# Kernel tuning notes

Measured on AMD Instinct MI355X. Metric: run time of the kernel, lower is better.

## Reference

```python
import jax, jax.numpy as jnp
import numpy as np

B, T, D, H, L = 8192, 80, 32, 64, 3


def setup_inputs() -> dict:
    key = jax.random.key(0)
    ks = jax.random.split(key, 16)
    s = lambda k, shape, fan: jax.random.normal(k, shape, jnp.float32) / np.sqrt(fan)
    inp = {"x": jax.random.normal(ks[0], (B, T, D), jnp.float32)}
    dims_in = [D, H, H]
    i = 1
    for l in range(L):
        din = dims_in[l]
        inp[f"W_ih{l}"] = s(ks[i], (H, din), H); i += 1
        inp[f"W_hh{l}"] = s(ks[i], (H, H), H); i += 1
        inp[f"b_ih{l}"] = s(ks[i], (H,), H); i += 1
        inp[f"b_hh{l}"] = s(ks[i], (H,), H); i += 1
    inp["W_fc"] = s(ks[i], (1, H), H); i += 1
    inp["b_fc"] = s(ks[i], (1,), H)
    return inp


def _rnn_layer(xs, W_ih, W_hh, b_ih, b_hh):
    # xs: [T, B, Din] -> ys: [T, B, H]; tanh RNN recurrence (PyTorch nn.RNN math)
    pre = jnp.einsum('tbd,hd->tbh', xs, W_ih) + b_ih + b_hh  # input proj precomputed
    h0 = jnp.zeros((xs.shape[1], W_hh.shape[0]), xs.dtype)
    def step(h, p):
        h_new = jnp.tanh(p + h @ W_hh.T)
        return h_new, h_new
    _, ys = jax.lax.scan(step, h0, pre)
    return ys


def reference(x, W_ih0, W_hh0, b_ih0, b_hh0, W_ih1, W_hh1, b_ih1, b_hh1,
              W_ih2, W_hh2, b_ih2, b_hh2, W_fc, b_fc):
    # x: [B, T, D] (batch_first) -> time-major [T, B, D]
    h = jnp.swapaxes(x, 0, 1)
    params = [(W_ih0, W_hh0, b_ih0, b_hh0),
              (W_ih1, W_hh1, b_ih1, b_hh1),
              (W_ih2, W_hh2, b_ih2, b_hh2)]
    for (W_ih, W_hh, b_ih, b_hh) in params:
        h = _rnn_layer(h, W_ih, W_hh, b_ih, b_hh)
    last = h[-1]                      # [B, H] == out[:, -1, :]
    return last @ W_fc.T + b_fc       # [B, 1]
```

## Files before the change

### kernel.cpp

```cpp
#include <hip/hip_runtime.h>
#include <hip/hip_bf16.h>
#include <cstddef>


typedef __attribute__((ext_vector_type(8))) short s16x8;
typedef __attribute__((ext_vector_type(4))) short s16x4;
typedef __attribute__((ext_vector_type(4))) float fx4;

#define MFMA16(A, B, C) __builtin_amdgcn_mfma_f32_16x16x32_bf16((A), (B), (C), 0, 0, 0)

#if __has_builtin(__builtin_amdgcn_exp2f)
#define EXP2F(x) __builtin_amdgcn_exp2f(x)
#else
#define EXP2F(x) exp2f(x)
#endif
#if __has_builtin(__builtin_amdgcn_rcpf)
#define RCPF(x) __builtin_amdgcn_rcpf(x)
#else
#define RCPF(x) (1.0f / (x))
#endif

static constexpr float K2LOG2E = 2.8853900817779268f;

__device__ __forceinline__ short f2bf(float f) {
  union { float f; unsigned u; } v; v.f = f;
  unsigned r = v.u + 0x7FFFu + ((v.u >> 16) & 1u);
  return (short)(r >> 16);
}
__device__ __forceinline__ float bf2f(short s) {
  union { unsigned u; float f; } v; v.u = ((unsigned)(unsigned short)s) << 16;
  return v.f;
}
__device__ __forceinline__ unsigned pk2bf(float a, float b) {
  float2 t; t.x = a; t.y = b;
  union { __hip_bfloat162 h; unsigned u; } c;
  c.h = __float22bfloat162_rn(t);
  return c.u;
}

__device__ __forceinline__ s16x8 wfragA(const float* W, int ncols, int row, int col0) {
  const float* p = W + row * ncols + col0;
  s16x8 r;
#pragma unroll
  for (int i = 0; i < 8; ++i) r[i] = f2bf(p[i]);
  return r;
}

__global__ __launch_bounds__(384, 3) void rnn3_pipe6(
    const float* __restrict__ x,
    const float* __restrict__ Wih0, const float* __restrict__ Whh0,
    const float* __restrict__ bih0, const float* __restrict__ bhh0,
    const float* __restrict__ Wih1, const float* __restrict__ Whh1,
    const float* __restrict__ bih1, const float* __restrict__ bhh1,
    const float* __restrict__ Wih2, const float* __restrict__ Whh2,
    const float* __restrict__ bih2, const float* __restrict__ bhh2,
    const float* __restrict__ Wfc, const float* __restrict__ bfc,
    float* __restrict__ out)
{
  __shared__ __align__(16) short hb[3][2][16][72];

  const int tid = threadIdx.x;
  const int wvu = __builtin_amdgcn_readfirstlane(tid >> 6);
  const int l   = wvu >> 1;
  const int s   = wvu & 1;
  const int ln  = tid & 63;
  const int q   = ln >> 4;
  const int m15 = ln & 15;
  const int bbase = (int)blockIdx.x * 16;

  const float* Wih = (l == 0) ? Wih0 : (l == 1) ? Wih1 : Wih2;
  const float* Whh = (l == 0) ? Whh0 : (l == 1) ? Whh1 : Whh2;
  const float* bi  = (l == 0) ? bih0 : (l == 1) ? bih1 : bih2;
  const float* bh  = (l == 0) ? bhh0 : (l == 1) ? bhh1 : bhh2;
  const int kin = (l == 0) ? 32 : 64;

  const s16x8 z8 = {0, 0, 0, 0, 0, 0, 0, 0};
  s16x8 wi0[2], wi1[2], whOwn[2], whOth[2];
#pragma unroll
  for (int tile = 0; tile < 2; ++tile) {
    const int row = 32 * s + 16 * tile + m15;
    wi0[tile]   = wfragA(Wih, kin, row, 8 * q);
    wi1[tile]   = l ? wfragA(Wih, 64, row, 32 + 8 * q) : z8;
    whOwn[tile] = wfragA(Whh, 64, row, 32 * s + 8 * q);
    whOth[tile] = wfragA(Whh, 64, row, 32 * (1 - s) + 8 * q);
  }

  float bsc[2][4];
#pragma unroll
  for (int tile = 0; tile < 2; ++tile)
#pragma unroll
    for (int r = 0; r < 4; ++r) {
      const int j = 32 * s + 16 * tile + 4 * q + r;
      bsc[tile][r] = (bi[j] + bh[j]) * K2LOG2E;
    }

  short*       wr_[2]  = {&hb[l][0][m15][32 * s + 4 * q], &hb[l][1][m15][32 * s + 4 * q]};
  const short* own_[2] = {&hb[l][0][m15][32 * s + 8 * q], &hb[l][1][m15][32 * s + 8 * q]};
  const short* oth_[2] = {&hb[l][0][m15][32 * (1 - s) + 8 * q],
                          &hb[l][1][m15][32 * (1 - s) + 8 * q]};
  const int lup = (l == 0) ? 0 : l - 1;
  const short* up_[2]  = {&hb[lup][0][m15][8 * q], &hb[lup][1][m15][8 * q]};

  const float* xr = x + (size_t)(bbase + m15) * (80 * 32) + 8 * q;
  fx4 xc0 = {0, 0, 0, 0}, xc1 = {0, 0, 0, 0};
  if (l == 0) { xc0 = *(const fx4*)(xr); xc1 = *(const fx4*)(xr + 4); }

  const fx4 z4 = {0.f, 0.f, 0.f, 0.f};
  s16x8 rOwn = z8;

  for (int tau = 0; tau < 82; ++tau) {
    const int lt = tau - l;
    if (0 <= lt && lt < 80) {
      const int p  = lt & 1;
      const int pm = p ^ 1;
      s16x8 rOth = z8;
      if (lt > 0) rOth = *(const s16x8*)(oth_[pm]);
      s16x8 in0, in1 = z8;
      if (l == 0) {
        union { unsigned u[4]; s16x8 v; } xp;
        xp.u[0] = pk2bf(xc0[0], xc0[1]); xp.u[1] = pk2bf(xc0[2], xc0[3]);
        xp.u[2] = pk2bf(xc1[0], xc1[1]); xp.u[3] = pk2bf(xc1[2], xc1[3]);
        in0 = xp.v;
        const int tn = (lt < 79) ? lt + 1 : 79;
        xc0 = *(const fx4*)(xr + tn * 32);
        xc1 = *(const fx4*)(xr + tn * 32 + 4);
      } else {
        const short* up = up_[p];
        in0 = *(const s16x8*)(up);
        in1 = *(const s16x8*)(up + 32);
      }
      fx4 acc[2];
#pragma unroll
      for (int tile = 0; tile < 2; ++tile) acc[tile] = MFMA16(whOwn[tile], rOwn, z4);
#pragma unroll
      for (int tile = 0; tile < 2; ++tile) acc[tile] = MFMA16(whOth[tile], rOth, acc[tile]);
#pragma unroll
      for (int tile = 0; tile < 2; ++tile) acc[tile] = MFMA16(wi0[tile], in0, acc[tile]);
      if (l) {
#pragma unroll
        for (int tile = 0; tile < 2; ++tile) acc[tile] = MFMA16(wi1[tile], in1, acc[tile]);
      }
      short* wb = wr_[p];
#pragma unroll
      for (int tile = 0; tile < 2; ++tile) {
        float h[4];
#pragma unroll
        for (int r = 0; r < 4; ++r) {
          float e = EXP2F(__builtin_fmaf(acc[tile][r], K2LOG2E, bsc[tile][r]));
          h[r] = __builtin_fmaf(-2.f, RCPF(e + 1.f), 1.f);
        }
        union { unsigned u[2]; s16x4 v; } pk;
        pk.u[0] = pk2bf(h[0], h[1]);
        pk.u[1] = pk2bf(h[2], h[3]);
        *(s16x4*)(wb + 16 * tile) = pk.v;
      }
      rOwn = *(const s16x8*)(own_[p]);
    }
    __syncthreads();
  }

  if (wvu == 4) {
    const short* f = &hb[2][1][m15][8 * q];
    s16x8 f0 = *(const s16x8*)(f);
    s16x8 f1 = *(const s16x8*)(f + 32);
    float sv = 0.f;
#pragma unroll
    for (int i = 0; i < 8; ++i) sv += bf2f(f0[i]) * Wfc[8 * q + i];
#pragma unroll
    for (int i = 0; i < 8; ++i) sv += bf2f(f1[i]) * Wfc[32 + 8 * q + i];
    sv += __shfl_xor(sv, 16, 64);
    sv += __shfl_xor(sv, 32, 64);
    if (ln < 16) out[bbase + ln] = sv + bfc[0];
  }
}

extern "C" void kernel_launch(void* const* d_in, const int* in_sizes, int n_in,
                              void* d_out, int out_size, void* d_ws, size_t ws_size,
                              hipStream_t stream) {
  const float* x    = (const float*)d_in[0];
  const float* Wih0 = (const float*)d_in[1];
  const float* Whh0 = (const float*)d_in[2];
  const float* bih0 = (const float*)d_in[3];
  const float* bhh0 = (const float*)d_in[4];
  const float* Wih1 = (const float*)d_in[5];
  const float* Whh1 = (const float*)d_in[6];
  const float* bih1 = (const float*)d_in[7];
  const float* bhh1 = (const float*)d_in[8];
  const float* Wih2 = (const float*)d_in[9];
  const float* Whh2 = (const float*)d_in[10];
  const float* bih2 = (const float*)d_in[11];
  const float* bhh2 = (const float*)d_in[12];
  const float* Wfc  = (const float*)d_in[13];
  const float* bfc  = (const float*)d_in[14];

  rnn3_pipe6<<<dim3(512), dim3(384), 0, stream>>>(
      x, Wih0, Whh0, bih0, bhh0, Wih1, Whh1, bih1, bhh1,
      Wih2, Whh2, bih2, bhh2, Wfc, bfc, (float*)d_out);
}
```

Measured before the change: 209.0 us.

## Run all three layers per wave in a wavefront-skewed systolic loop

Each wave used to own one layer's half of the hidden state. Now each wave holds the weights for all three layers and computes every layer's output columns for its half, skewed in time so layer l handles step tau-l. A block covers two 16-row batch groups with 256 threads, and the grid drops to 256 blocks with launch bounds (256,1). The final FC dot is fused in from register-held layer-2 outputs and reduced through shared memory. The aim is to fill each wave's serial dependency chain with independent MFMAs from other layers. The cost is much higher register pressure and fewer resident waves, which may leave the latency of the recurrence exposed.

```diff
diff --git a/kernel.cpp b/kernel.cpp
--- a/kernel.cpp
+++ b/kernel.cpp
@@ -27,10 +27,6 @@
   unsigned r = v.u + 0x7FFFu + ((v.u >> 16) & 1u);
   return (short)(r >> 16);
 }
-__device__ __forceinline__ float bf2f(short s) {
-  union { unsigned u; float f; } v; v.u = ((unsigned)(unsigned short)s) << 16;
-  return v.f;
-}
 __device__ __forceinline__ unsigned pk2bf(float a, float b) {
   float2 t; t.x = a; t.y = b;
   union { __hip_bfloat162 h; unsigned u; } c;
@@ -46,7 +42,22 @@
   return r;
 }
 
-__global__ __launch_bounds__(384, 3) void rnn3_pipe6(
+__device__ __forceinline__ void tanh_pack_store(const fx4 acc, const float* bs,
+                                                short* wp, float* hout) {
+  float h[4];
+#pragma unroll
+  for (int r = 0; r < 4; ++r) {
+    float e = EXP2F(__builtin_fmaf(acc[r], K2LOG2E, bs[r]));
+    h[r] = __builtin_fmaf(-2.f, RCPF(e + 1.f), 1.f);
+    if (hout) hout[r] = h[r];
+  }
+  union { unsigned u[2]; s16x4 v; } pk;
+  pk.u[0] = pk2bf(h[0], h[1]);
+  pk.u[1] = pk2bf(h[2], h[3]);
+  *(s16x4*)wp = pk.v;
+}
+
+__global__ __launch_bounds__(256, 1) void rnn3_sys(
     const float* __restrict__ x,
     const float* __restrict__ Wih0, const float* __restrict__ Whh0,
     const float* __restrict__ bih0, const float* __restrict__ bhh0,
@@ -57,121 +68,131 @@
     const float* __restrict__ Wfc, const float* __restrict__ bfc,
     float* __restrict__ out)
 {
-  __shared__ __align__(16) short hb[3][2][16][72];
+  __shared__ __align__(16) short hb[2][3][2][16][72];
 
   const int tid = threadIdx.x;
   const int wvu = __builtin_amdgcn_readfirstlane(tid >> 6);
-  const int l   = wvu >> 1;
+  const int g   = wvu >> 1;
   const int s   = wvu & 1;
   const int ln  = tid & 63;
   const int q   = ln >> 4;
   const int m15 = ln & 15;
-  const int bbase = (int)blockIdx.x * 16;
-
-  const float* Wih = (l == 0) ? Wih0 : (l == 1) ? Wih1 : Wih2;
-  const float* Whh = (l == 0) ? Whh0 : (l == 1) ? Whh1 : Whh2;
-  const float* bi  = (l == 0) ? bih0 : (l == 1) ? bih1 : bih2;
-  const float* bh  = (l == 0) ? bhh0 : (l == 1) ? bhh1 : bhh2;
-  const int kin = (l == 0) ? 32 : 64;
-
-  const s16x8 z8 = {0, 0, 0, 0, 0, 0, 0, 0};
-  s16x8 wi0[2], wi1[2], whOwn[2], whOth[2];
+  const int bbase = (int)blockIdx.x * 32 + g * 16;
+
+  {
+    const s16x8 z = {0, 0, 0, 0, 0, 0, 0, 0};
+    s16x8* pz = (s16x8*)&hb[0][0][0][0][0];
+    for (int i = tid; i < (int)(sizeof(hb) / 16); i += 256) pz[i] = z;
+  }
+
+  s16x8 wi0[2], wh0[2][2], wi1[2][2], wh1[2][2], wi2[2][2], wh2[2][2];
 #pragma unroll
   for (int tile = 0; tile < 2; ++tile) {
     const int row = 32 * s + 16 * tile + m15;
-    wi0[tile]   = wfragA(Wih, kin, row, 8 * q);
-    wi1[tile]   = l ? wfragA(Wih, 64, row, 32 + 8 * q) : z8;
-    whOwn[tile] = wfragA(Whh, 64, row, 32 * s + 8 * q);
-    whOth[tile] = wfragA(Whh, 64, row, 32 * (1 - s) + 8 * q);
-  }
-
-  float bsc[2][4];
+    wi0[tile] = wfragA(Wih0, 32, row, 8 * q);
+#pragma unroll
+    for (int kf = 0; kf < 2; ++kf) {
+      const int c = 32 * kf + 8 * q;
+      wh0[tile][kf] = wfragA(Whh0, 64, row, c);
+      wi1[tile][kf] = wfragA(Wih1, 64, row, c);
+      wh1[tile][kf] = wfragA(Whh1, 64, row, c);
+      wi2[tile][kf] = wfragA(Wih2, 64, row, c);
+      wh2[tile][kf] = wfragA(Whh2, 64, row, c);
+    }
+  }
+
+  float bs[3][2][4];
 #pragma unroll
   for (int tile = 0; tile < 2; ++tile)
 #pragma unroll
     for (int r = 0; r < 4; ++r) {
       const int j = 32 * s + 16 * tile + 4 * q + r;
-      bsc[tile][r] = (bi[j] + bh[j]) * K2LOG2E;
-    }
-
-  short*       wr_[2]  = {&hb[l][0][m15][32 * s + 4 * q], &hb[l][1][m15][32 * s + 4 * q]};
-  const short* own_[2] = {&hb[l][0][m15][32 * s + 8 * q], &hb[l][1][m15][32 * s + 8 * q]};
-  const short* oth_[2] = {&hb[l][0][m15][32 * (1 - s) + 8 * q],
-                          &hb[l][1][m15][32 * (1 - s) + 8 * q]};
-  const int lup = (l == 0) ? 0 : l - 1;
-  const short* up_[2]  = {&hb[lup][0][m15][8 * q], &hb[lup][1][m15][8 * q]};
+      bs[0][tile][r] = (bih0[j] + bhh0[j]) * K2LOG2E;
+      bs[1][tile][r] = (bih1[j] + bhh1[j]) * K2LOG2E;
+      bs[2][tile][r] = (bih2[j] + bhh2[j]) * K2LOG2E;
+    }
+
+  short* wrp[3][2];
+  const short* rdp[3][2];
+#pragma unroll
+  for (int l = 0; l < 3; ++l)
+#pragma unroll
+    for (int p = 0; p < 2; ++p) {
+      wrp[l][p] = &hb[g][l][p][m15][32 * s + 4 * q];
+      rdp[l][p] = &hb[g][l][p][m15][8 * q];
+    }
 
   const float* xr = x + (size_t)(bbase + m15) * (80 * 32) + 8 * q;
-  fx4 xc0 = {0, 0, 0, 0}, xc1 = {0, 0, 0, 0};
-  if (l == 0) { xc0 = *(const fx4*)(xr); xc1 = *(const fx4*)(xr + 4); }
+  fx4 xa = *(const fx4*)(xr);
+  fx4 xb = *(const fx4*)(xr + 4);
 
   const fx4 z4 = {0.f, 0.f, 0.f, 0.f};
-  s16x8 rOwn = z8;
+  float hk2[2][4];
+
+  __syncthreads();
 
   for (int tau = 0; tau < 82; ++tau) {
-    const int lt = tau - l;
-    if (0 <= lt && lt < 80) {
-      const int p  = lt & 1;
-      const int pm = p ^ 1;
-      s16x8 rOth = z8;
-      if (lt > 0) rOth = *(const s16x8*)(oth_[pm]);
-      s16x8 in0, in1 = z8;
-      if (l == 0) {
-        union { unsigned u[4]; s16x8 v; } xp;
-        xp.u[0] = pk2bf(xc0[0], xc0[1]); xp.u[1] = pk2bf(xc0[2], xc0[3]);
-        xp.u[2] = pk2bf(xc1[0], xc1[1]); xp.u[3] = pk2bf(xc1[2], xc1[3]);
-        in0 = xp.v;
-        const int tn = (lt < 79) ? lt + 1 : 79;
-        xc0 = *(const fx4*)(xr + tn * 32);
-        xc1 = *(const fx4*)(xr + tn * 32 + 4);
-      } else {
-        const short* up = up_[p];
-        in0 = *(const s16x8*)(up);
-        in1 = *(const s16x8*)(up + 32);
+    const int p  = tau & 1;
+    const int pm = p ^ 1;
+
+    s16x8 h0a = *(const s16x8*)(rdp[0][pm]);
+    s16x8 h0b = *(const s16x8*)(rdp[0][pm] + 32);
+    s16x8 h1a = *(const s16x8*)(rdp[1][pm]);
+    s16x8 h1b = *(const s16x8*)(rdp[1][pm] + 32);
+    s16x8 h2a = *(const s16x8*)(rdp[2][pm]);
+    s16x8 h2b = *(const s16x8*)(rdp[2][pm] + 32);
+
+    if (tau <= 79) {
+      union { unsigned u[4]; s16x8 v; } xp;
+      xp.u[0] = pk2bf(xa[0], xa[1]); xp.u[1] = pk2bf(xa[2], xa[3]);
+      xp.u[2] = pk2bf(xb[0], xb[1]); xp.u[3] = pk2bf(xb[2], xb[3]);
+      const int tn = (tau < 79) ? tau + 1 : 79;
+      xa = *(const fx4*)(xr + tn * 32);
+      xb = *(const fx4*)(xr + tn * 32 + 4);
+#pragma unroll
+      for (int tile = 0; tile < 2; ++tile) {
+        fx4 a = MFMA16(wi0[tile], xp.v, z4);
+        a = MFMA16(wh0[tile][0], h0a, a);
+        a = MFMA16(wh0[tile][1], h0b, a);
+        tanh_pack_store(a, bs[0][tile], wrp[0][p] + 16 * tile, nullptr);
       }
-      fx4 acc[2];
-#pragma unroll
-      for (int tile = 0; tile < 2; ++tile) acc[tile] = MFMA16(whOwn[tile], rOwn, z4);
-#pragma unroll
-      for (int tile = 0; tile < 2; ++tile) acc[tile] = MFMA16(whOth[tile], rOth, acc[tile]);
-#pragma unroll
-      for (int tile = 0; tile < 2; ++tile) acc[tile] = MFMA16(wi0[tile], in0, acc[tile]);
-      if (l) {
-#pragma unroll
-        for (int tile = 0; tile < 2; ++tile) acc[tile] = MFMA16(wi1[tile], in1, acc[tile]);
+    }
+    if (1 <= tau && tau <= 80) {
+#pragma unroll
+      for (int tile = 0; tile < 2; ++tile) {
+        fx4 a = MFMA16(wi1[tile][0], h0a, z4);
+        a = MFMA16(wi1[tile][1], h0b, a);
+        a = MFMA16(wh1[tile][0], h1a, a);
+        a = MFMA16(wh1[tile][1], h1b, a);
+        tanh_pack_store(a, bs[1][tile], wrp[1][p] + 16 * tile, nullptr);
       }
-      short* wb = wr_[p];
+    }
+    if (tau >= 2) {
 #pragma unroll
       for (int tile = 0; tile < 2; ++tile) {
-        float h[4];
-#pragma unroll
-        for (int r = 0; r < 4; ++r) {
-          float e = EXP2F(__builtin_fmaf(acc[tile][r], K2LOG2E, bsc[tile][r]));
-          h[r] = __builtin_fmaf(-2.f, RCPF(e + 1.f), 1.f);
-        }
-        union { unsigned u[2]; s16x4 v; } pk;
-        pk.u[0] = pk2bf(h[0], h[1]);
-        pk.u[1] = pk2bf(h[2], h[3]);
-        *(s16x4*)(wb + 16 * tile) = pk.v;
+        fx4 a = MFMA16(wi2[tile][0], h1a, z4);
+        a = MFMA16(wi2[tile][1], h1b, a);
+        a = MFMA16(wh2[tile][0], h2a, a);
+        a = MFMA16(wh2[tile][1], h2b, a);
+        tanh_pack_store(a, bs[2][tile], wrp[2][p] + 16 * tile, hk2[tile]);
       }
-      rOwn = *(const s16x8*)(own_[p]);
     }
     __syncthreads();
   }
 
-  if (wvu == 4) {
-    const short* f = &hb[2][1][m15][8 * q];
-    s16x8 f0 = *(const s16x8*)(f);
-    s16x8 f1 = *(const s16x8*)(f + 32);
-    float sv = 0.f;
-#pragma unroll
-    for (int i = 0; i < 8; ++i) sv += bf2f(f0[i]) * Wfc[8 * q + i];
-#pragma unroll
-    for (int i = 0; i < 8; ++i) sv += bf2f(f1[i]) * Wfc[32 + 8 * q + i];
-    sv += __shfl_xor(sv, 16, 64);
-    sv += __shfl_xor(sv, 32, 64);
-    if (ln < 16) out[bbase + ln] = sv + bfc[0];
-  }
+  float sv = 0.f;
+#pragma unroll
+  for (int tile = 0; tile < 2; ++tile)
+#pragma unroll
+    for (int r = 0; r < 4; ++r)
+      sv += hk2[tile][r] * Wfc[32 * s + 16 * tile + 4 * q + r];
+  sv += __shfl_xor(sv, 16, 64);
+  sv += __shfl_xor(sv, 32, 64);
+  float* fcb = (float*)&hb[0][0][0][0][0];
+  if (ln < 16) fcb[(g * 2 + s) * 16 + ln] = sv;
+  __syncthreads();
+  if (s == 0 && ln < 16)
+    out[bbase + ln] = fcb[(g * 2 + 0) * 16 + ln] + fcb[(g * 2 + 1) * 16 + ln] + bfc[0];
 }
 
 extern "C" void kernel_launch(void* const* d_in, const int* in_sizes, int n_in,
@@ -193,7 +214,7 @@
   const float* Wfc  = (const float*)d_in[13];
   const float* bfc  = (const float*)d_in[14];
 
-  rnn3_pipe6<<<dim3(512), dim3(384), 0, stream>>>(
+  rnn3_sys<<<dim3(256), dim3(256), 0, stream>>>(
       x, Wih0, Whh0, bih0, bhh0, Wih1, Whh1, bih1, bhh1,
       Wih2, Whh2, bih2, bhh2, Wfc, bfc, (float*)d_out);
 }
```

Result: slower. 240.0 us (+14.8%).

## Run all three RNN layers in one register-resident wave with 16x16x16 MFMA

Applied to the files above, without the earlier changes.

Replaces the six-wave layer/half-split pipeline, which passed hidden states through LDS with a block barrier every step, with a single wave per 16-row batch tile. That wave computes all three layers sequentially each timestep. It switches the recurrent and inter-layer products to the 16x16x16 bf16 MFMA, whose output fragment layout matches its B-operand layout, so tanh outputs feed the next MFMA straight from registers with no LDS traffic or synchronisation. The cost is a much longer serial MFMA chain per wave, all weights held in VGPRs, and only one wave per block, so far fewer waves per CU are left to hide latency.

```diff
diff --git a/kernel.cpp b/kernel.cpp
--- a/kernel.cpp
+++ b/kernel.cpp
@@ -7,7 +7,8 @@
 typedef __attribute__((ext_vector_type(4))) short s16x4;
 typedef __attribute__((ext_vector_type(4))) float fx4;
 
-#define MFMA16(A, B, C) __builtin_amdgcn_mfma_f32_16x16x32_bf16((A), (B), (C), 0, 0, 0)
+#define MFMA32(A, B, C) __builtin_amdgcn_mfma_f32_16x16x32_bf16((A), (B), (C), 0, 0, 0)
+#define MFMA16(A, B, C) __builtin_amdgcn_mfma_f32_16x16x16bf16_1k((A), (B), (C), 0, 0, 0)
 
 #if __has_builtin(__builtin_amdgcn_exp2f)
 #define EXP2F(x) __builtin_amdgcn_exp2f(x)
@@ -38,7 +39,14 @@
   return c.u;
 }
 
-__device__ __forceinline__ s16x8 wfragA(const float* W, int ncols, int row, int col0) {
+__device__ __forceinline__ s16x4 wfragA16(const float* W, int ncols, int row, int col0) {
+  const float* p = W + row * ncols + col0;
+  s16x4 r;
+#pragma unroll
+  for (int i = 0; i < 4; ++i) r[i] = f2bf(p[i]);
+  return r;
+}
+__device__ __forceinline__ s16x8 wfragA32(const float* W, int ncols, int row, int col0) {
   const float* p = W + row * ncols + col0;
   s16x8 r;
 #pragma unroll
@@ -46,7 +54,20 @@
   return r;
 }
 
-__global__ __launch_bounds__(384, 3) void rnn3_pipe6(
+__device__ __forceinline__ s16x4 tanh_pack(fx4 acc, const float* bs) {
+  float h[4];
+#pragma unroll
+  for (int r = 0; r < 4; ++r) {
+    float e = EXP2F(__builtin_fmaf(acc[r], K2LOG2E, bs[r]));
+    h[r] = __builtin_fmaf(-2.f, RCPF(e + 1.f), 1.f);
+  }
+  union { unsigned u[2]; s16x4 v; } p;
+  p.u[0] = pk2bf(h[0], h[1]);
+  p.u[1] = pk2bf(h[2], h[3]);
+  return p.v;
+}
+
+__global__ __launch_bounds__(64, 1) void rnn3_k16(
     const float* __restrict__ x,
     const float* __restrict__ Wih0, const float* __restrict__ Whh0,
     const float* __restrict__ bih0, const float* __restrict__ bhh0,
@@ -57,121 +78,104 @@
     const float* __restrict__ Wfc, const float* __restrict__ bfc,
     float* __restrict__ out)
 {
-  __shared__ __align__(16) short hb[3][2][16][72];
-
-  const int tid = threadIdx.x;
-  const int wvu = __builtin_amdgcn_readfirstlane(tid >> 6);
-  const int l   = wvu >> 1;
-  const int s   = wvu & 1;
-  const int ln  = tid & 63;
-  const int q   = ln >> 4;
+  const int ln  = threadIdx.x & 63;
+  const int Q   = ln >> 4;
   const int m15 = ln & 15;
   const int bbase = (int)blockIdx.x * 16;
 
-  const float* Wih = (l == 0) ? Wih0 : (l == 1) ? Wih1 : Wih2;
-  const float* Whh = (l == 0) ? Whh0 : (l == 1) ? Whh1 : Whh2;
-  const float* bi  = (l == 0) ? bih0 : (l == 1) ? bih1 : bih2;
-  const float* bh  = (l == 0) ? bhh0 : (l == 1) ? bhh1 : bhh2;
-  const int kin = (l == 0) ? 32 : 64;
-
-  const s16x8 z8 = {0, 0, 0, 0, 0, 0, 0, 0};
-  s16x8 wi0[2], wi1[2], whOwn[2], whOth[2];
-#pragma unroll
-  for (int tile = 0; tile < 2; ++tile) {
-    const int row = 32 * s + 16 * tile + m15;
-    wi0[tile]   = wfragA(Wih, kin, row, 8 * q);
-    wi1[tile]   = l ? wfragA(Wih, 64, row, 32 + 8 * q) : z8;
-    whOwn[tile] = wfragA(Whh, 64, row, 32 * s + 8 * q);
-    whOth[tile] = wfragA(Whh, 64, row, 32 * (1 - s) + 8 * q);
+  s16x8 wx[4];
+#pragma unroll
+  for (int t4 = 0; t4 < 4; ++t4) wx[t4] = wfragA32(Wih0, 32, 16 * t4 + m15, 8 * Q);
+  s16x4 wh0[4][4], wi1[4][4], wh1[4][4], wi2[4][4], wh2[4][4];
+#pragma unroll
+  for (int t4 = 0; t4 < 4; ++t4) {
+    const int row = 16 * t4 + m15;
+#pragma unroll
+    for (int kf = 0; kf < 4; ++kf) {
+      const int c = 16 * kf + 4 * Q;
+      wh0[t4][kf] = wfragA16(Whh0, 64, row, c);
+      wi1[t4][kf] = wfragA16(Wih1, 64, row, c);
+      wh1[t4][kf] = wfragA16(Whh1, 64, row, c);
+      wi2[t4][kf] = wfragA16(Wih2, 64, row, c);
+      wh2[t4][kf] = wfragA16(Whh2, 64, row, c);
+    }
   }
 
-  float bsc[2][4];
-#pragma unroll
-  for (int tile = 0; tile < 2; ++tile)
+  float bs0[4][4], bs1[4][4], bs2[4][4];
+#pragma unroll
+  for (int t4 = 0; t4 < 4; ++t4)
 #pragma unroll
     for (int r = 0; r < 4; ++r) {
-      const int j = 32 * s + 16 * tile + 4 * q + r;
-      bsc[tile][r] = (bi[j] + bh[j]) * K2LOG2E;
+      const int j = 16 * t4 + 4 * Q + r;
+      bs0[t4][r] = (bih0[j] + bhh0[j]) * K2LOG2E;
+      bs1[t4][r] = (bih1[j] + bhh1[j]) * K2LOG2E;
+      bs2[t4][r] = (bih2[j] + bhh2[j]) * K2LOG2E;
     }
 
-  short*       wr_[2]  = {&hb[l][0][m15][32 * s + 4 * q], &hb[l][1][m15][32 * s + 4 * q]};
-  const short* own_[2] = {&hb[l][0][m15][32 * s + 8 * q], &hb[l][1][m15][32 * s + 8 * q]};
-  const short* oth_[2] = {&hb[l][0][m15][32 * (1 - s) + 8 * q],
-                          &hb[l][1][m15][32 * (1 - s) + 8 * q]};
-  const int lup = (l == 0) ? 0 : l - 1;
-  const short* up_[2]  = {&hb[lup][0][m15][8 * q], &hb[lup][1][m15][8 * q]};
-
-  const float* xr = x + (size_t)(bbase + m15) * (80 * 32) + 8 * q;
-  fx4 xc0 = {0, 0, 0, 0}, xc1 = {0, 0, 0, 0};
-  if (l == 0) { xc0 = *(const fx4*)(xr); xc1 = *(const fx4*)(xr + 4); }
-
+  const s16x4 z2 = {0, 0, 0, 0};
+  s16x4 h0f[4] = {z2, z2, z2, z2};
+  s16x4 h1f[4] = {z2, z2, z2, z2};
+  s16x4 h2f[4] = {z2, z2, z2, z2};
   const fx4 z4 = {0.f, 0.f, 0.f, 0.f};
-  s16x8 rOwn = z8;
-
-  for (int tau = 0; tau < 82; ++tau) {
-    const int lt = tau - l;
-    if (0 <= lt && lt < 80) {
-      const int p  = lt & 1;
-      const int pm = p ^ 1;
-      s16x8 rOth = z8;
-      if (lt > 0) rOth = *(const s16x8*)(oth_[pm]);
-      s16x8 in0, in1 = z8;
-      if (l == 0) {
-        union { unsigned u[4]; s16x8 v; } xp;
-        xp.u[0] = pk2bf(xc0[0], xc0[1]); xp.u[1] = pk2bf(xc0[2], xc0[3]);
-        xp.u[2] = pk2bf(xc1[0], xc1[1]); xp.u[3] = pk2bf(xc1[2], xc1[3]);
-        in0 = xp.v;
-        const int tn = (lt < 79) ? lt + 1 : 79;
-        xc0 = *(const fx4*)(xr + tn * 32);
-        xc1 = *(const fx4*)(xr + tn * 32 + 4);
-      } else {
-        const short* up = up_[p];
-        in0 = *(const s16x8*)(up);
-        in1 = *(const s16x8*)(up + 32);
-      }
-      fx4 acc[2];
-#pragma unroll
-      for (int tile = 0; tile < 2; ++tile) acc[tile] = MFMA16(whOwn[tile], rOwn, z4);
-#pragma unroll
-      for (int tile = 0; tile < 2; ++tile) acc[tile] = MFMA16(whOth[tile], rOth, acc[tile]);
-#pragma unroll
-      for (int tile = 0; tile < 2; ++tile) acc[tile] = MFMA16(wi0[tile], in0, acc[tile]);
-      if (l) {
-#pragma unroll
-        for (int tile = 0; tile < 2; ++tile) acc[tile] = MFMA16(wi1[tile], in1, acc[tile]);
-      }
-      short* wb = wr_[p];
-#pragma unroll
-      for (int tile = 0; tile < 2; ++tile) {
-        float h[4];
-#pragma unroll
-        for (int r = 0; r < 4; ++r) {
-          float e = EXP2F(__builtin_fmaf(acc[tile][r], K2LOG2E, bsc[tile][r]));
-          h[r] = __builtin_fmaf(-2.f, RCPF(e + 1.f), 1.f);
-        }
-        union { unsigned u[2]; s16x4 v; } pk;
-        pk.u[0] = pk2bf(h[0], h[1]);
-        pk.u[1] = pk2bf(h[2], h[3]);
-        *(s16x4*)(wb + 16 * tile) = pk.v;
-      }
-      rOwn = *(const s16x8*)(own_[p]);
-    }
-    __syncthreads();
+
+  const float* xr = x + (size_t)(bbase + m15) * (80 * 32) + 8 * Q;
+  fx4 xc0 = *(const fx4*)(xr);
+  fx4 xc1 = *(const fx4*)(xr + 4);
+
+  for (int t = 0; t < 80; ++t) {
+    union { unsigned u[4]; s16x8 v; } xp;
+    xp.u[0] = pk2bf(xc0[0], xc0[1]); xp.u[1] = pk2bf(xc0[2], xc0[3]);
+    xp.u[2] = pk2bf(xc1[0], xc1[1]); xp.u[3] = pk2bf(xc1[2], xc1[3]);
+    const int tn = (t < 79) ? t + 1 : 79;
+    xc0 = *(const fx4*)(xr + tn * 32);
+    xc1 = *(const fx4*)(xr + tn * 32 + 4);
+
+    fx4 a[4];
+#pragma unroll
+    for (int t4 = 0; t4 < 4; ++t4) a[t4] = MFMA32(wx[t4], xp.v, z4);
+#pragma unroll
+    for (int kf = 0; kf < 4; ++kf)
+#pragma unroll
+      for (int t4 = 0; t4 < 4; ++t4) a[t4] = MFMA16(wh0[t4][kf], h0f[kf], a[t4]);
+#pragma unroll
+    for (int t4 = 0; t4 < 4; ++t4) h0f[t4] = tanh_pack(a[t4], bs0[t4]);
+
+#pragma unroll
+    for (int t4 = 0; t4 < 4; ++t4) a[t4] = MFMA16(wi1[t4][0], h0f[0], z4);
+#pragma unroll
+    for (int kf = 1; kf < 4; ++kf)
+#pragma unroll
+      for (int t4 = 0; t4 < 4; ++t4) a[t4] = MFMA16(wi1[t4][kf], h0f[kf], a[t4]);
+#pragma unroll
+    for (int kf = 0; kf < 4; ++kf)
+#pragma unroll
+      for (int t4 = 0; t4 < 4; ++t4) a[t4] = MFMA16(wh1[t4][kf], h1f[kf], a[t4]);
+#pragma unroll
+    for (int t4 = 0; t4 < 4; ++t4) h1f[t4] = tanh_pack(a[t4], bs1[t4]);
+
+#pragma unroll
+    for (int t4 = 0; t4 < 4; ++t4) a[t4] = MFMA16(wi2[t4][0], h1f[0], z4);
+#pragma unroll
+    for (int kf = 1; kf < 4; ++kf)
+#pragma unroll
+      for (int t4 = 0; t4 < 4; ++t4) a[t4] = MFMA16(wi2[t4][kf], h1f[kf], a[t4]);
+#pragma unroll
+    for (int kf = 0; kf < 4; ++kf)
+#pragma unroll
+      for (int t4 = 0; t4 < 4; ++t4) a[t4] = MFMA16(wh2[t4][kf], h2f[kf], a[t4]);
+#pragma unroll
+    for (int t4 = 0; t4 < 4; ++t4) h2f[t4] = tanh_pack(a[t4], bs2[t4]);
   }
 
-  if (wvu == 4) {
-    const short* f = &hb[2][1][m15][8 * q];
-    s16x8 f0 = *(const s16x8*)(f);
-    s16x8 f1 = *(const s16x8*)(f + 32);
-    float sv = 0.f;
-#pragma unroll
-    for (int i = 0; i < 8; ++i) sv += bf2f(f0[i]) * Wfc[8 * q + i];
-#pragma unroll
-    for (int i = 0; i < 8; ++i) sv += bf2f(f1[i]) * Wfc[32 + 8 * q + i];
-    sv += __shfl_xor(sv, 16, 64);
-    sv += __shfl_xor(sv, 32, 64);
-    if (ln < 16) out[bbase + ln] = sv + bfc[0];
-  }
+  float sv = 0.f;
+#pragma unroll
+  for (int kf = 0; kf < 4; ++kf)
+#pragma unroll
+    for (int i = 0; i < 4; ++i)
+      sv += bf2f(h2f[kf][i]) * Wfc[16 * kf + 4 * Q + i];
+  sv += __shfl_xor(sv, 16, 64);
+  sv += __shfl_xor(sv, 32, 64);
+  if (ln < 16) out[bbase + ln] = sv + bfc[0];
 }
 
 extern "C" void kernel_launch(void* const* d_in, const int* in_sizes, int n_in,
@@ -193,7 +197,7 @@
   const float* Wfc  = (const float*)d_in[13];
   const float* bfc  = (const float*)d_in[14];
 
-  rnn3_pipe6<<<dim3(512), dim3(384), 0, stream>>>(
+  rnn3_k16<<<dim3(512), dim3(64), 0, stream>>>(
       x, Wih0, Whh0, bih0, bhh0, Wih1, Whh1, bih1, bhh1,
       Wih2, Whh2, bih2, bhh2, Wfc, bfc, (float*)d_out);
 }
```

Measured after the change: 235.2 us. 1.13x slower.
